# Kernel optimization log

Measured on AMD Instinct MI355X. Metric: run time of the kernel, lower is better.

The kernel has to match this reference:

```python
import jax, jax.numpy as jnp
import numpy as np

D = 1024      # model_dim
H = 16        # n_heads
BLOCK = 256   # block_dim
B, S = 4, 4096


def setup_inputs() -> dict:
    key = jax.random.key(0)
    ks = jax.random.split(key, 6)
    x = jax.random.normal(ks[0], (B, S, D), dtype=jnp.float32)
    # random permutation per batch row (mirrors torch.argsort(torch.rand(...)))
    rand_perm = jnp.argsort(jax.random.uniform(ks[1], (B, S)), axis=-1).astype(jnp.int32)
    W_in = jax.random.normal(ks[2], (D, 3 * D), dtype=jnp.float32) / np.float32(np.sqrt(D))
    b_in = jax.random.normal(ks[3], (3 * D,), dtype=jnp.float32) * 0.02
    W_out = jax.random.normal(ks[4], (D, D), dtype=jnp.float32) / np.float32(np.sqrt(D))
    b_out = jax.random.normal(ks[5], (D,), dtype=jnp.float32) * 0.02
    return {"x": x, "rand_perm": rand_perm, "W_in": W_in, "b_in": b_in,
            "W_out": W_out, "b_out": b_out}


def reference(x, rand_perm, W_in, b_in, W_out, b_out):
    Bb, Ss, Dm = x.shape
    dh = Dm // H
    nb = Ss // BLOCK  # S divisible by BLOCK -> no padding needed
    # permute sequence: x_rand[..., i, :] = x[..., perm[i], :]
    x_r = jnp.take_along_axis(x, rand_perm[..., None], axis=-2)          # [B,S,D]
    xb = x_r.reshape(Bb, nb, BLOCK, Dm)                                   # block-diagonal chunks
    qkv = jnp.einsum('bntd,de->bnte', xb, W_in) + b_in                    # [B,nb,blk,3D]
    # torch layout: chunk by head first, then (q,k,v) within head
    qkv = qkv.reshape(Bb, nb, BLOCK, H, 3, dh)
    q = jnp.moveaxis(qkv[..., 0, :], 3, 2)                                # [B,nb,H,blk,dh]
    k = jnp.moveaxis(qkv[..., 1, :], 3, 2)
    v = jnp.moveaxis(qkv[..., 2, :], 3, 2)
    scores = jnp.einsum('bnhtd,bnhsd->bnhts', q, k) / np.float32(np.sqrt(dh))
    att = jax.nn.softmax(scores, axis=-1)
    o = jnp.einsum('bnhts,bnhsd->bnhtd', att, v)                          # [B,nb,H,blk,dh]

    def merge(t):  # [B,nb,H,blk,dh] -> [B,S,D] (heads concatenated on feature dim)
        return jnp.moveaxis(t, 2, 3).reshape(Bb, Ss, Dm)

    o = merge(o) @ W_out + b_out
    k_f = merge(k)
    v_f = merge(v)
    # scatter back: out[perm[i]] = src[i]  <=>  out[j] = src[inv_perm[j]]
    inv = jnp.argsort(rand_perm, axis=-1)
    unperm = lambda t: jnp.take_along_axis(t, inv[..., None], axis=-2)
    return unperm(o), unperm(k_f), unperm(v_f)
```

## Files before the change

kernel.cpp:

```cpp
#include <hip/hip_runtime.h>

#define D_   1024
#define H_   16
#define DHd  64
#define BLK  256
#define B_   4
#define S_   4096
#define NB_  16
#define M_   16384
#define N1_  3072

typedef __attribute__((ext_vector_type(8))) short short8;
typedef __attribute__((ext_vector_type(4))) float f32x4;
typedef unsigned short u16;
typedef __attribute__((ext_vector_type(4))) unsigned short u16x4;

__device__ inline u16 f2bf(float f) {
  unsigned int u = __float_as_uint(f);
  unsigned int r = (u + 0x7fffu + ((u >> 16) & 1u)) >> 16;
  return (u16)r;
}

__device__ inline void async_ld16(const void* g, void* l) {
  __builtin_amdgcn_global_load_lds(
      (const __attribute__((address_space(1))) unsigned int*)g,
      (__attribute__((address_space(3))) unsigned int*)l, 16, 0, 0);
}

__global__ __launch_bounds__(256)
void permute_cast_kernel(const float* __restrict__ x, const int* __restrict__ perm,
                         u16* __restrict__ xp) {
  int bid = blockIdx.x;
  int b = bid >> 12;
  int i = bid & 4095;
  int prow = perm[b * S_ + i];
  const float4* src = reinterpret_cast<const float4*>(x + (size_t)(b * S_ + prow) * D_);
  float4 v = src[threadIdx.x];
  u16x4 o;
  o.x = f2bf(v.x); o.y = f2bf(v.y); o.z = f2bf(v.z); o.w = f2bf(v.w);
  reinterpret_cast<u16x4*>(xp + (size_t)bid * D_)[threadIdx.x] = o;
}

__global__ __launch_bounds__(256)
void transpose_cast_kernel(const float* __restrict__ src, u16* __restrict__ dst,
                           int R, int C) {
  __shared__ float tile[32][33];
  int tx = threadIdx.x, ty = threadIdx.y;
  int c0 = blockIdx.x * 32, r0 = blockIdx.y * 32;
  #pragma unroll
  for (int i = ty; i < 32; i += 8)
    tile[i][tx] = src[(size_t)(r0 + i) * C + c0 + tx];
  __syncthreads();
  #pragma unroll
  for (int i = ty; i < 32; i += 8)
    dst[(size_t)(c0 + i) * R + r0 + tx] = f2bf(tile[tx][i]);
}

template<int MODE>
__global__ __launch_bounds__(256)
void gemm_kernel(const u16* __restrict__ A, const u16* __restrict__ BT,
                 const float* __restrict__ bias, const int* __restrict__ perm,
                 u16* __restrict__ q_ws, u16* __restrict__ k_ws, u16* __restrict__ vT_ws,
                 float* __restrict__ out_k, float* __restrict__ out_v,
                 float* __restrict__ out_o) {
  __shared__ u16 Al[128 * 32];
  __shared__ u16 Bl[128 * 32];
  __shared__ int perm_l[128];

  const int tid  = threadIdx.x;
  const int lane = tid & 63;
  const int w    = tid >> 6;
  const int wm   = w >> 1, wn = w & 1;
  const int i0   = blockIdx.x * 128;
  const int n0   = blockIdx.y * 128;
  const int bidx = i0 >> 12;
  const int l4   = lane >> 4;
  const int l15  = lane & 15;
  const int lr   = lane >> 2;
  const int lk   = (lane & 3) << 3;

  if (tid < 128) perm_l[tid] = perm[bidx * S_ + (i0 & 4095) + tid];

  f32x4 acc[4][4] = {};

  #pragma unroll 2
  for (int kt = 0; kt < 1024; kt += 32) {
    #pragma unroll
    for (int c = 0; c < 2; ++c) {
      int rA = w * 32 + c * 16;
      async_ld16(A  + (size_t)(i0 + rA + lr) * 1024 + kt + lk, &Al[rA * 32]);
      async_ld16(BT + (size_t)(n0 + rA + lr) * 1024 + kt + lk, &Bl[rA * 32]);
    }
    __syncthreads();
    short8 af[4], bf[4];
    #pragma unroll
    for (int mt = 0; mt < 4; ++mt)
      af[mt] = *reinterpret_cast<const short8*>(&Al[(wm * 64 + mt * 16 + l15) * 32 + l4 * 8]);
    #pragma unroll
    for (int nt = 0; nt < 4; ++nt)
      bf[nt] = *reinterpret_cast<const short8*>(&Bl[(wn * 64 + nt * 16 + l15) * 32 + l4 * 8]);
    #pragma unroll
    for (int mt = 0; mt < 4; ++mt)
      #pragma unroll
      for (int nt = 0; nt < 4; ++nt)
        acc[mt][nt] = __builtin_amdgcn_mfma_f32_16x16x32_bf16(af[mt], bf[nt], acc[mt][nt], 0, 0, 0);
    __syncthreads();
  }

  if (MODE == 0) {
    #pragma unroll
    for (int nt = 0; nt < 4; ++nt) {
      int col = n0 + wn * 64 + nt * 16 + l15;
      float bias_v = bias[col];
      int h  = col / 192;
      int rem = col - h * 192;
      int cc = rem >> 6;
      int dd = rem & 63;
      int qcol = (h << 6) + dd;
      #pragma unroll
      for (int mt = 0; mt < 4; ++mt) {
        int rbase = i0 + wm * 64 + mt * 16 + l4 * 4;
        if (cc == 0) {
          #pragma unroll
          for (int r = 0; r < 4; ++r) {
            float val = acc[mt][nt][r] + bias_v;
            q_ws[(size_t)(rbase + r) * D_ + qcol] = f2bf(val);
          }
        } else if (cc == 1) {
          #pragma unroll
          for (int r = 0; r < 4; ++r) {
            float val = acc[mt][nt][r] + bias_v;
            int rr = rbase + r;
            k_ws[(size_t)rr * D_ + qcol] = f2bf(val);
            int prow = perm_l[rr - i0];
            out_k[(size_t)(bidx * S_ + prow) * D_ + qcol] = val;
          }
        } else {
          u16x4 pk;
          #pragma unroll
          for (int r = 0; r < 4; ++r) {
            float val = acc[mt][nt][r] + bias_v;
            int rr = rbase + r;
            int prow = perm_l[rr - i0];
            out_v[(size_t)(bidx * S_ + prow) * D_ + qcol] = val;
            pk[r] = f2bf(val);
          }
          int i_loc = rbase & 4095;
          int nblk = i_loc >> 8;
          int t    = i_loc & 255;
          *reinterpret_cast<u16x4*>(
              &vT_ws[((((size_t)bidx * NB_ + nblk) * H_ + h) * DHd + dd) * BLK + t]) = pk;
        }
      }
    }
  } else {
    #pragma unroll
    for (int nt = 0; nt < 4; ++nt) {
      int col = n0 + wn * 64 + nt * 16 + l15;
      float bias_v = bias[col];
      #pragma unroll
      for (int mt = 0; mt < 4; ++mt) {
        int rbase = i0 + wm * 64 + mt * 16 + l4 * 4;
        #pragma unroll
        for (int r = 0; r < 4; ++r) {
          int rr = rbase + r;
          int prow = perm_l[rr - i0];
          out_o[(size_t)(bidx * S_ + prow) * D_ + col] = acc[mt][nt][r] + bias_v;
        }
      }
    }
  }
}

__global__ __launch_bounds__(256)
void attn_kernel(const u16* __restrict__ q_ws, const u16* __restrict__ k_ws,
                 const u16* __restrict__ vT_ws, u16* __restrict__ o_ws) {
  __shared__ u16 P_lds[4 * 64 * 64];

  int bid  = blockIdx.x;
  int h    = bid & 15;
  int nblk = (bid >> 4) & 15;
  int b    = bid >> 8;
  int row0 = b * S_ + nblk * BLK;
  int lane = threadIdx.x & 63;
  int w    = threadIdx.x >> 6;
  int l4 = lane >> 4, l15 = lane & 15;

  const u16* qb  = q_ws + (size_t)row0 * D_ + h * 64;
  const u16* kb  = k_ws + (size_t)row0 * D_ + h * 64;
  const u16* vTb = vT_ws + ((size_t)(b * NB_ + nblk) * H_ + h) * (size_t)(DHd * BLK);

  short8 qf[4][2];
  #pragma unroll
  for (int mt = 0; mt < 4; ++mt)
    #pragma unroll
    for (int kk = 0; kk < 2; ++kk)
      qf[mt][kk] = *reinterpret_cast<const short8*>(
          qb + (size_t)(w * 64 + mt * 16 + l15) * D_ + kk * 32 + l4 * 8);

  f32x4 Oacc[4][4] = {};
  float mS[4][4], lS[4][4];
  #pragma unroll
  for (int mt = 0; mt < 4; ++mt)
    #pragma unroll
    for (int r = 0; r < 4; ++r) { mS[mt][r] = -1e30f; lS[mt][r] = 0.f; }

  for (int ct = 0; ct < 4; ++ct) {
    f32x4 Sc[4][4] = {};
    #pragma unroll
    for (int kk = 0; kk < 2; ++kk) {
      #pragma unroll
      for (int nt = 0; nt < 4; ++nt) {
        short8 kf = *reinterpret_cast<const short8*>(
            kb + (size_t)(ct * 64 + nt * 16 + l15) * D_ + kk * 32 + l4 * 8);
        #pragma unroll
        for (int mt = 0; mt < 4; ++mt)
          Sc[mt][nt] = __builtin_amdgcn_mfma_f32_16x16x32_bf16(qf[mt][kk], kf, Sc[mt][nt], 0, 0, 0);
      }
    }
    #pragma unroll
    for (int mt = 0; mt < 4; ++mt) {
      #pragma unroll
      for (int r = 0; r < 4; ++r) {
        float v0 = fmaxf(fmaxf(Sc[mt][0][r], Sc[mt][1][r]), fmaxf(Sc[mt][2][r], Sc[mt][3][r]));
        v0 *= 0.125f;
        v0 = fmaxf(v0, __shfl_xor(v0, 1));
        v0 = fmaxf(v0, __shfl_xor(v0, 2));
        v0 = fmaxf(v0, __shfl_xor(v0, 4));
        v0 = fmaxf(v0, __shfl_xor(v0, 8));
        float mn = fmaxf(mS[mt][r], v0);
        float alpha = __expf(mS[mt][r] - mn);
        mS[mt][r] = mn;
        float rs = 0.f;
        #pragma unroll
        for (int nt = 0; nt < 4; ++nt) {
          float p = __expf(Sc[mt][nt][r] * 0.125f - mn);
          Sc[mt][nt][r] = p;
          rs += p;
        }
        rs += __shfl_xor(rs, 1);
        rs += __shfl_xor(rs, 2);
        rs += __shfl_xor(rs, 4);
        rs += __shfl_xor(rs, 8);
        lS[mt][r] = lS[mt][r] * alpha + rs;
        #pragma unroll
        for (int nt = 0; nt < 4; ++nt)
          Oacc[mt][nt][r] *= alpha;
      }
    }
    #pragma unroll
    for (int mt = 0; mt < 4; ++mt)
      #pragma unroll
      for (int nt = 0; nt < 4; ++nt)
        #pragma unroll
        for (int r = 0; r < 4; ++r)
          P_lds[w * 4096 + (mt * 16 + l4 * 4 + r) * 64 + nt * 16 + l15] = f2bf(Sc[mt][nt][r]);
    #pragma unroll
    for (int kk = 0; kk < 2; ++kk) {
      short8 pa[4];
      #pragma unroll
      for (int mt = 0; mt < 4; ++mt)
        pa[mt] = *reinterpret_cast<const short8*>(
            &P_lds[w * 4096 + (mt * 16 + l15) * 64 + kk * 32 + l4 * 8]);
      #pragma unroll
      for (int nt = 0; nt < 4; ++nt) {
        short8 vf = *reinterpret_cast<const short8*>(
            vTb + (size_t)(nt * 16 + l15) * BLK + ct * 64 + kk * 32 + l4 * 8);
        #pragma unroll
        for (int mt = 0; mt < 4; ++mt)
          Oacc[mt][nt] = __builtin_amdgcn_mfma_f32_16x16x32_bf16(pa[mt], vf, Oacc[mt][nt], 0, 0, 0);
      }
    }
  }
  u16* ob = o_ws + (size_t)row0 * D_ + h * 64;
  #pragma unroll
  for (int mt = 0; mt < 4; ++mt)
    #pragma unroll
    for (int r = 0; r < 4; ++r) {
      float inv = 1.f / lS[mt][r];
      int row = w * 64 + mt * 16 + l4 * 4 + r;
      #pragma unroll
      for (int nt = 0; nt < 4; ++nt)
        ob[(size_t)row * D_ + nt * 16 + l15] = f2bf(Oacc[mt][nt][r] * inv);
    }
}

extern "C" void kernel_launch(void* const* d_in, const int* in_sizes, int n_in,
                              void* d_out, int out_size, void* d_ws, size_t ws_size,
                              hipStream_t stream) {
  const float* x     = (const float*)d_in[0];
  const int*   perm  = (const int*)d_in[1];
  const float* W_in  = (const float*)d_in[2];
  const float* b_in  = (const float*)d_in[3];
  const float* W_out = (const float*)d_in[4];
  const float* b_out = (const float*)d_in[5];

  float* out_o = (float*)d_out;
  float* out_k = out_o + (size_t)M_ * D_;
  float* out_v = out_k + (size_t)M_ * D_;

  const size_t nE = (size_t)M_ * D_;
  u16 *xp, *q_ws, *k_ws, *vT, *o_ws, *WinT, *WoutT;
  size_t need_full = (5 * nE + (size_t)N1_ * D_ + (size_t)D_ * D_) * 2;
  if (ws_size >= need_full) {
    u16* w = (u16*)d_ws;
    xp = w; q_ws = xp + nE; k_ws = q_ws + nE; vT = k_ws + nE; o_ws = vT + nE;
    WinT = o_ws + nE; WoutT = WinT + (size_t)N1_ * D_;
  } else {
    xp = (u16*)d_out; q_ws = xp + nE;
    u16* w = (u16*)d_ws;
    k_ws = w; vT = k_ws + nE; o_ws = vT + nE;
    WinT = o_ws + nE; WoutT = WinT + (size_t)N1_ * D_;
  }

  permute_cast_kernel<<<M_, 256, 0, stream>>>(x, perm, xp);
  transpose_cast_kernel<<<dim3(N1_ / 32, D_ / 32), dim3(32, 8), 0, stream>>>(W_in, WinT, D_, N1_);
  transpose_cast_kernel<<<dim3(D_ / 32, D_ / 32), dim3(32, 8), 0, stream>>>(W_out, WoutT, D_, D_);
  gemm_kernel<0><<<dim3(M_ / 128, N1_ / 128), 256, 0, stream>>>(
      xp, WinT, b_in, perm, q_ws, k_ws, vT, out_k, out_v, nullptr);
  attn_kernel<<<B_ * NB_ * H_, 256, 0, stream>>>(q_ws, k_ws, vT, o_ws);
  gemm_kernel<1><<<dim3(M_ / 128, D_ / 128), 256, 0, stream>>>(
      o_ws, WoutT, b_out, perm, nullptr, nullptr, nullptr, nullptr, nullptr, out_o);
}
```

Baseline: 387.1 us.

## Rewrite GEMM as 256x256-tile, 512-thread, 4-stage async-pipelined MFMA kernel

The projection GEMMs move from 128x128 tiles with 256 threads and a single-buffered load/sync loop to 256x256 tiles with 512 threads. Each k-slice is staged into a 4-deep LDS ring with async global-to-LDS loads issued two iterations ahead, and waits use explicit vmcnt counts. The LDS layout uses an XOR swizzle to avoid bank conflicts, MFMA runs are wrapped in s_setprio, and the block index is remapped so neighbouring workgroups share tiles across XCDs. The aim is to hide global-memory latency and raise operand reuse. The cost is 128KB of LDS per block and more accumulator registers per thread, which may limit occupancy or cause spills.

Measured after the change: 322.8 us. 1.2x faster.

```diff
diff --git a/kernel.cpp b/kernel.cpp
--- a/kernel.cpp
+++ b/kernel.cpp
@@ -9,6 +9,7 @@
 #define NB_  16
 #define M_   16384
 #define N1_  3072
+#define NT_  32
 
 typedef __attribute__((ext_vector_type(8))) short short8;
 typedef __attribute__((ext_vector_type(4))) float f32x4;
@@ -57,60 +58,103 @@
 }
 
 template<int MODE>
-__global__ __launch_bounds__(256)
+__global__ __launch_bounds__(512, 2)
 void gemm_kernel(const u16* __restrict__ A, const u16* __restrict__ BT,
                  const float* __restrict__ bias, const int* __restrict__ perm,
                  u16* __restrict__ q_ws, u16* __restrict__ k_ws, u16* __restrict__ vT_ws,
                  float* __restrict__ out_k, float* __restrict__ out_v,
                  float* __restrict__ out_o) {
-  __shared__ u16 Al[128 * 32];
-  __shared__ u16 Bl[128 * 32];
-  __shared__ int perm_l[128];
+  constexpr int NCOL = (MODE == 0) ? N1_ : D_;
+  constexpr int NWG  = (M_ / 256) * (NCOL / 256);
+  constexpr int CPX  = NWG / 8;
+
+  __shared__ u16 LDS[4 * 16384];
+  __shared__ int perm_l[256];
 
   const int tid  = threadIdx.x;
   const int lane = tid & 63;
   const int w    = tid >> 6;
-  const int wm   = w >> 1, wn = w & 1;
-  const int i0   = blockIdx.x * 128;
-  const int n0   = blockIdx.y * 128;
+  const int wr   = w >> 2, wc = w & 3;
+  const int l4   = lane >> 4, l15 = lane & 15;
+
+  const int orig = blockIdx.x;
+  const int lid  = (orig & 7) * CPX + (orig >> 3);
+  const int i0   = (lid & 63) * 256;
+  const int n0   = (lid >> 6) * 256;
   const int bidx = i0 >> 12;
-  const int l4   = lane >> 4;
-  const int l15  = lane & 15;
-  const int lr   = lane >> 2;
-  const int lk   = (lane & 3) << 3;
-
-  if (tid < 128) perm_l[tid] = perm[bidx * S_ + (i0 & 4095) + tid];
-
-  f32x4 acc[4][4] = {};
-
-  #pragma unroll 2
-  for (int kt = 0; kt < 1024; kt += 32) {
-    #pragma unroll
-    for (int c = 0; c < 2; ++c) {
-      int rA = w * 32 + c * 16;
-      async_ld16(A  + (size_t)(i0 + rA + lr) * 1024 + kt + lk, &Al[rA * 32]);
-      async_ld16(BT + (size_t)(n0 + rA + lr) * 1024 + kt + lk, &Bl[rA * 32]);
-    }
-    __syncthreads();
-    short8 af[4], bf[4];
-    #pragma unroll
-    for (int mt = 0; mt < 4; ++mt)
-      af[mt] = *reinterpret_cast<const short8*>(&Al[(wm * 64 + mt * 16 + l15) * 32 + l4 * 8]);
-    #pragma unroll
-    for (int nt = 0; nt < 4; ++nt)
-      bf[nt] = *reinterpret_cast<const short8*>(&Bl[(wn * 64 + nt * 16 + l15) * 32 + l4 * 8]);
-    #pragma unroll
-    for (int mt = 0; mt < 4; ++mt)
-      #pragma unroll
-      for (int nt = 0; nt < 4; ++nt)
-        acc[mt][nt] = __builtin_amdgcn_mfma_f32_16x16x32_bf16(af[mt], bf[nt], acc[mt][nt], 0, 0, 0);
-    __syncthreads();
+
+  if (tid < 256) perm_l[tid] = perm[bidx * S_ + (i0 & 4095) + tid];
+
+  const int srow = tid >> 2;
+  const int sq   = (tid & 3) ^ ((tid >> 3) & 3);
+  const u16* pA0 = A  + (size_t)(i0 + srow) * 1024 + sq * 8;
+  const u16* pA1 = pA0 + (size_t)128 * 1024;
+  const u16* pB0 = BT + (size_t)(n0 + srow) * 1024 + sq * 8;
+  const u16* pB1 = pB0 + (size_t)128 * 1024;
+
+  const int ps   = l4 ^ ((l15 >> 1) & 3);
+  const int aoff = (wr * 128 + l15) * 64 + ps * 16;
+  const int boff = 16384 + (wc * 64 + l15) * 64 + ps * 16;
+
+  f32x4 acc[8][4] = {};
+
+  #define STAGE(kt, b) do {                                    \
+    const int ko_ = (kt) * 32;                                 \
+    u16* base_ = &LDS[(b) * 16384 + w * 512];                  \
+    async_ld16(pA0 + ko_, base_);                              \
+    async_ld16(pA1 + ko_, base_ + 4096);                       \
+    async_ld16(pB0 + ko_, base_ + 8192);                       \
+    async_ld16(pB1 + ko_, base_ + 12288);                      \
+  } while (0)
+
+  #define COMPUTE(b) do {                                                         \
+    const char* lb_ = (const char*)LDS + (b) * 32768;                             \
+    short8 af_[8], bf_[4];                                                        \
+    _Pragma("unroll")                                                             \
+    for (int m = 0; m < 8; ++m)                                                   \
+      af_[m] = *reinterpret_cast<const short8*>(lb_ + aoff + m * 1024);           \
+    bf_[0] = *reinterpret_cast<const short8*>(lb_ + boff);                        \
+    bf_[1] = *reinterpret_cast<const short8*>(lb_ + boff + 1024);                 \
+    __builtin_amdgcn_s_setprio(1);                                                \
+    _Pragma("unroll")                                                             \
+    for (int m = 0; m < 8; ++m) {                                                 \
+      acc[m][0] = __builtin_amdgcn_mfma_f32_16x16x32_bf16(af_[m], bf_[0], acc[m][0], 0, 0, 0); \
+      acc[m][1] = __builtin_amdgcn_mfma_f32_16x16x32_bf16(af_[m], bf_[1], acc[m][1], 0, 0, 0); \
+    }                                                                             \
+    __builtin_amdgcn_s_setprio(0);                                                \
+    bf_[2] = *reinterpret_cast<const short8*>(lb_ + boff + 2048);                 \
+    bf_[3] = *reinterpret_cast<const short8*>(lb_ + boff + 3072);                 \
+    __builtin_amdgcn_s_setprio(1);                                                \
+    _Pragma("unroll")                                                             \
+    for (int m = 0; m < 8; ++m) {                                                 \
+      acc[m][2] = __builtin_amdgcn_mfma_f32_16x16x32_bf16(af_[m], bf_[2], acc[m][2], 0, 0, 0); \
+      acc[m][3] = __builtin_amdgcn_mfma_f32_16x16x32_bf16(af_[m], bf_[3], acc[m][3], 0, 0, 0); \
+    }                                                                             \
+    __builtin_amdgcn_s_setprio(0);                                                \
+  } while (0)
+
+  STAGE(0, 0);
+  STAGE(1, 1);
+  #pragma unroll 1
+  for (int kt = 0; kt < NT_ - 2; ++kt) {
+    STAGE(kt + 2, (kt + 2) & 3);
+    asm volatile("s_waitcnt vmcnt(8) lgkmcnt(0)" ::: "memory");
+    __builtin_amdgcn_s_barrier();
+    COMPUTE(kt & 3);
   }
+  asm volatile("s_waitcnt vmcnt(4) lgkmcnt(0)" ::: "memory");
+  __builtin_amdgcn_s_barrier();
+  COMPUTE((NT_ - 2) & 3);
+  asm volatile("s_waitcnt vmcnt(0) lgkmcnt(0)" ::: "memory");
+  __builtin_amdgcn_s_barrier();
+  COMPUTE((NT_ - 1) & 3);
+  #undef STAGE
+  #undef COMPUTE
 
   if (MODE == 0) {
     #pragma unroll
-    for (int nt = 0; nt < 4; ++nt) {
-      int col = n0 + wn * 64 + nt * 16 + l15;
+    for (int n = 0; n < 4; ++n) {
+      int col = n0 + wc * 64 + n * 16 + l15;
       float bias_v = bias[col];
       int h  = col / 192;
       int rem = col - h * 192;
@@ -118,18 +162,18 @@
       int dd = rem & 63;
       int qcol = (h << 6) + dd;
       #pragma unroll
-      for (int mt = 0; mt < 4; ++mt) {
-        int rbase = i0 + wm * 64 + mt * 16 + l4 * 4;
+      for (int m = 0; m < 8; ++m) {
+        int rbase = i0 + wr * 128 + m * 16 + l4 * 4;
         if (cc == 0) {
           #pragma unroll
           for (int r = 0; r < 4; ++r) {
-            float val = acc[mt][nt][r] + bias_v;
+            float val = acc[m][n][r] + bias_v;
             q_ws[(size_t)(rbase + r) * D_ + qcol] = f2bf(val);
           }
         } else if (cc == 1) {
           #pragma unroll
           for (int r = 0; r < 4; ++r) {
-            float val = acc[mt][nt][r] + bias_v;
+            float val = acc[m][n][r] + bias_v;
             int rr = rbase + r;
             k_ws[(size_t)rr * D_ + qcol] = f2bf(val);
             int prow = perm_l[rr - i0];
@@ -139,7 +183,7 @@
           u16x4 pk;
           #pragma unroll
           for (int r = 0; r < 4; ++r) {
-            float val = acc[mt][nt][r] + bias_v;
+            float val = acc[m][n][r] + bias_v;
             int rr = rbase + r;
             int prow = perm_l[rr - i0];
             out_v[(size_t)(bidx * S_ + prow) * D_ + qcol] = val;
@@ -155,17 +199,17 @@
     }
   } else {
     #pragma unroll
-    for (int nt = 0; nt < 4; ++nt) {
-      int col = n0 + wn * 64 + nt * 16 + l15;
+    for (int n = 0; n < 4; ++n) {
+      int col = n0 + wc * 64 + n * 16 + l15;
       float bias_v = bias[col];
       #pragma unroll
-      for (int mt = 0; mt < 4; ++mt) {
-        int rbase = i0 + wm * 64 + mt * 16 + l4 * 4;
+      for (int m = 0; m < 8; ++m) {
+        int rbase = i0 + wr * 128 + m * 16 + l4 * 4;
         #pragma unroll
         for (int r = 0; r < 4; ++r) {
           int rr = rbase + r;
           int prow = perm_l[rr - i0];
-          out_o[(size_t)(bidx * S_ + prow) * D_ + col] = acc[mt][nt][r] + bias_v;
+          out_o[(size_t)(bidx * S_ + prow) * D_ + col] = acc[m][n][r] + bias_v;
         }
       }
     }
@@ -316,9 +360,9 @@
   permute_cast_kernel<<<M_, 256, 0, stream>>>(x, perm, xp);
   transpose_cast_kernel<<<dim3(N1_ / 32, D_ / 32), dim3(32, 8), 0, stream>>>(W_in, WinT, D_, N1_);
   transpose_cast_kernel<<<dim3(D_ / 32, D_ / 32), dim3(32, 8), 0, stream>>>(W_out, WoutT, D_, D_);
-  gemm_kernel<0><<<dim3(M_ / 128, N1_ / 128), 256, 0, stream>>>(
+  gemm_kernel<0><<<(M_ / 256) * (N1_ / 256), 512, 0, stream>>>(
       xp, WinT, b_in, perm, q_ws, k_ws, vT, out_k, out_v, nullptr);
   attn_kernel<<<B_ * NB_ * H_, 256, 0, stream>>>(q_ws, k_ws, vT, o_ws);
-  gemm_kernel<1><<<dim3(M_ / 128, D_ / 128), 256, 0, stream>>>(
+  gemm_kernel<1><<<(M_ / 256) * (D_ / 256), 512, 0, stream>>>(
       o_ws, WoutT, b_out, perm, nullptr, nullptr, nullptr, nullptr, nullptr, out_o);
 }
```

## Swizzle GEMM LDS layout, remap workgroups per XCD, and cap registers for occupancy

Applied to the files above, without the earlier changes.

The GEMM kernels now use a 1D grid whose block IDs are remapped so that consecutive tiles land on the same XCD (blocks are distributed round-robin across 8 XCDs), which improves L2 reuse of the A and B panels. The shared-memory staging uses an XOR-swizzled layout so the short8 fragment reads avoid LDS bank conflicts, with precomputed global pointers. Launch bounds request 3 waves per SIMD to raise occupancy, at the risk of register spills in the 4x4 MFMA accumulator tile.

Result: faster. 346.9 us (-10.4%).

```diff
diff --git a/kernel.cpp b/kernel.cpp
--- a/kernel.cpp
+++ b/kernel.cpp
@@ -9,6 +9,7 @@
 #define NB_  16
 #define M_   16384
 #define N1_  3072
+#define NT_  32
 
 typedef __attribute__((ext_vector_type(8))) short short8;
 typedef __attribute__((ext_vector_type(4))) float f32x4;
@@ -57,48 +58,66 @@
 }
 
 template<int MODE>
-__global__ __launch_bounds__(256)
+__global__ __launch_bounds__(256, 3)
 void gemm_kernel(const u16* __restrict__ A, const u16* __restrict__ BT,
                  const float* __restrict__ bias, const int* __restrict__ perm,
                  u16* __restrict__ q_ws, u16* __restrict__ k_ws, u16* __restrict__ vT_ws,
                  float* __restrict__ out_k, float* __restrict__ out_v,
                  float* __restrict__ out_o) {
-  __shared__ u16 Al[128 * 32];
-  __shared__ u16 Bl[128 * 32];
+  constexpr int NCOL = (MODE == 0) ? N1_ : D_;
+  constexpr int NPAN = NCOL / 128;
+  constexpr int NWG  = (M_ / 128) * NPAN;
+  constexpr int CPX  = NWG / 8;
+
+  __shared__ u16 LDS[8192];
   __shared__ int perm_l[128];
 
   const int tid  = threadIdx.x;
   const int lane = tid & 63;
   const int w    = tid >> 6;
   const int wm   = w >> 1, wn = w & 1;
-  const int i0   = blockIdx.x * 128;
-  const int n0   = blockIdx.y * 128;
+  const int l4   = lane >> 4, l15 = lane & 15;
+
+  const int orig = blockIdx.x;
+  const int lid  = (orig & 7) * CPX + (orig >> 3);
+  const int i0   = (lid / NPAN) * 128;
+  const int n0   = (lid % NPAN) * 128;
   const int bidx = i0 >> 12;
-  const int l4   = lane >> 4;
-  const int l15  = lane & 15;
-  const int lr   = lane >> 2;
-  const int lk   = (lane & 3) << 3;
 
   if (tid < 128) perm_l[tid] = perm[bidx * S_ + (i0 & 4095) + tid];
 
+  const int srow = (w << 4) + (lane >> 2);
+  const int sq   = (lane & 3) ^ ((lane >> 3) & 3);
+  const u16* pA0 = A  + (size_t)(i0 + srow) * 1024 + sq * 8;
+  const u16* pA1 = pA0 + (size_t)64 * 1024;
+  const u16* pB0 = BT + (size_t)(n0 + srow) * 1024 + sq * 8;
+  const u16* pB1 = pB0 + (size_t)64 * 1024;
+
+  const int ps   = l4 ^ ((l15 >> 1) & 3);
+  const int aoff = (wm * 64 + l15) * 64 + ps * 16;
+  const int boff = 8192 + (wn * 64 + l15) * 64 + ps * 16;
+
   f32x4 acc[4][4] = {};
 
   #pragma unroll 2
-  for (int kt = 0; kt < 1024; kt += 32) {
-    #pragma unroll
-    for (int c = 0; c < 2; ++c) {
-      int rA = w * 32 + c * 16;
-      async_ld16(A  + (size_t)(i0 + rA + lr) * 1024 + kt + lk, &Al[rA * 32]);
-      async_ld16(BT + (size_t)(n0 + rA + lr) * 1024 + kt + lk, &Bl[rA * 32]);
+  for (int kt = 0; kt < NT_; ++kt) {
+    {
+      const int ko = kt * 32;
+      u16* dA = &LDS[w * 512];
+      async_ld16(pA0 + ko, dA);
+      async_ld16(pA1 + ko, dA + 2048);
+      async_ld16(pB0 + ko, dA + 4096);
+      async_ld16(pB1 + ko, dA + 6144);
     }
     __syncthreads();
     short8 af[4], bf[4];
+    const char* lb = (const char*)LDS;
     #pragma unroll
     for (int mt = 0; mt < 4; ++mt)
-      af[mt] = *reinterpret_cast<const short8*>(&Al[(wm * 64 + mt * 16 + l15) * 32 + l4 * 8]);
+      af[mt] = *reinterpret_cast<const short8*>(lb + aoff + mt * 1024);
     #pragma unroll
     for (int nt = 0; nt < 4; ++nt)
-      bf[nt] = *reinterpret_cast<const short8*>(&Bl[(wn * 64 + nt * 16 + l15) * 32 + l4 * 8]);
+      bf[nt] = *reinterpret_cast<const short8*>(lb + boff + nt * 1024);
     #pragma unroll
     for (int mt = 0; mt < 4; ++mt)
       #pragma unroll
@@ -122,10 +141,8 @@
         int rbase = i0 + wm * 64 + mt * 16 + l4 * 4;
         if (cc == 0) {
           #pragma unroll
-          for (int r = 0; r < 4; ++r) {
-            float val = acc[mt][nt][r] + bias_v;
-            q_ws[(size_t)(rbase + r) * D_ + qcol] = f2bf(val);
-          }
+          for (int r = 0; r < 4; ++r)
+            q_ws[(size_t)(rbase + r) * D_ + qcol] = f2bf(acc[mt][nt][r] + bias_v);
         } else if (cc == 1) {
           #pragma unroll
           for (int r = 0; r < 4; ++r) {
@@ -316,9 +333,9 @@
   permute_cast_kernel<<<M_, 256, 0, stream>>>(x, perm, xp);
   transpose_cast_kernel<<<dim3(N1_ / 32, D_ / 32), dim3(32, 8), 0, stream>>>(W_in, WinT, D_, N1_);
   transpose_cast_kernel<<<dim3(D_ / 32, D_ / 32), dim3(32, 8), 0, stream>>>(W_out, WoutT, D_, D_);
-  gemm_kernel<0><<<dim3(M_ / 128, N1_ / 128), 256, 0, stream>>>(
+  gemm_kernel<0><<<(M_ / 128) * (N1_ / 128), 256, 0, stream>>>(
       xp, WinT, b_in, perm, q_ws, k_ws, vT, out_k, out_v, nullptr);
   attn_kernel<<<B_ * NB_ * H_, 256, 0, stream>>>(q_ws, k_ws, vT, o_ws);
-  gemm_kernel<1><<<dim3(M_ / 128, D_ / 128), 256, 0, stream>>>(
+  gemm_kernel<1><<<(M_ / 128) * (D_ / 128), 256, 0, stream>>>(
       o_ws, WoutT, b_out, perm, nullptr, nullptr, nullptr, nullptr, nullptr, out_o);
 }
```
